# Performance work log

Hardware: AMD Instinct MI355X
Metric: run time of the kernel (lower is better)

Reference implementation:

```python
import jax, jax.numpy as jnp
import numpy as np

VOCAB = 1_000_000
TOTAL = 819_200
BATCH = 16_384
DIM = 16


def setup_inputs() -> dict:
    key = jax.random.key(0)
    k1, k2, k3, k4 = jax.random.split(key, 4)
    feature_ids = jax.random.randint(k1, (TOTAL,), 0, VOCAB, dtype=jnp.int64 if jax.config.jax_enable_x64 else jnp.int32)
    feature_ratings = jax.random.uniform(k2, (TOTAL,), dtype=jnp.float32)
    segment_ids = jnp.sort(jax.random.randint(k3, (TOTAL,), 0, BATCH))
    weight = jax.random.normal(k4, (VOCAB, DIM), dtype=jnp.float32)
    bias = jnp.zeros((DIM,), dtype=jnp.float32)
    return {
        "feature_ids": feature_ids,
        "feature_ratings": feature_ratings,
        "segment_ids": segment_ids,
        "batch_size": BATCH,
        "weight": weight,
        "bias": bias,
    }


def reference(feature_ids, feature_ratings, segment_ids, batch_size, weight, bias):
    # gather rows [total, D], weight by per-token rating, ragged segment sum
    rows = weight[feature_ids] * feature_ratings[:, None]
    summed = jax.ops.segment_sum(rows, segment_ids, num_segments=batch_size,
                                 indices_are_sorted=True)
    return summed + bias  # [batch, D]
```

## Files before the change

### kernel.cpp

```cpp
#include <hip/hip_runtime.h>

#define DIM 16
#define CHUNK 4
#define NCHUNK 8
#define K_TOK (CHUNK * NCHUNK)

__global__ void init_out_kernel(float4* __restrict__ out4,
                                const float* __restrict__ bias,
                                int n4) {
    int i = blockIdx.x * blockDim.x + threadIdx.x;
    if (i < n4) {
        int d = (i & 3) * 4;
        out4[i] = make_float4(bias[d], bias[d + 1], bias[d + 2], bias[d + 3]);
    }
}

__global__ __launch_bounds__(256) void features_linear_kernel(
    const int*   __restrict__ ids,
    const float* __restrict__ ratings,
    const int*   __restrict__ segs,
    const float* __restrict__ weight,
    float*       __restrict__ out,
    int total) {
    int tid = blockIdx.x * blockDim.x + threadIdx.x;
    int d = tid & (DIM - 1);
    int stream_id = tid >> 4;
    int t0 = stream_id * K_TOK;
    if (t0 >= total) return;

    float acc = 0.0f;
    int prev = segs[t0];

    if (t0 + K_TOK <= total) {
        const int4*   idv = (const int4*)(ids + t0);
        const float4* rv  = (const float4*)(ratings + t0);
        const int4*   sv  = (const int4*)(segs + t0);

        int4   id = idv[0];
        float4 r  = rv[0];
        int4   s  = sv[0];

        #pragma unroll
        for (int c = 0; c < NCHUNK; ++c) {
            float w0 = weight[(size_t)id.x * DIM + d];
            float w1 = weight[(size_t)id.y * DIM + d];
            float w2 = weight[(size_t)id.z * DIM + d];
            float w3 = weight[(size_t)id.w * DIM + d];

            int4 nid; float4 nr; int4 ns;
            if (c + 1 < NCHUNK) {
                nid = idv[c + 1];
                nr  = rv[c + 1];
                ns  = sv[c + 1];
            }

            if (s.x != prev) { atomicAdd(&out[prev * DIM + d], acc); acc = 0.0f; prev = s.x; }
            acc = fmaf(w0, r.x, acc);
            if (s.y != prev) { atomicAdd(&out[prev * DIM + d], acc); acc = 0.0f; prev = s.y; }
            acc = fmaf(w1, r.y, acc);
            if (s.z != prev) { atomicAdd(&out[prev * DIM + d], acc); acc = 0.0f; prev = s.z; }
            acc = fmaf(w2, r.z, acc);
            if (s.w != prev) { atomicAdd(&out[prev * DIM + d], acc); acc = 0.0f; prev = s.w; }
            acc = fmaf(w3, r.w, acc);

            id = nid; r = nr; s = ns;
        }
    } else {
        int tend = total;
        for (int t = t0; t < tend; ++t) {
            int seg = segs[t];
            if (seg != prev) {
                atomicAdd(&out[prev * DIM + d], acc);
                acc = 0.0f;
                prev = seg;
            }
            acc = fmaf(weight[(size_t)ids[t] * DIM + d], ratings[t], acc);
        }
    }
    atomicAdd(&out[prev * DIM + d], acc);
}

extern "C" void kernel_launch(void* const* d_in, const int* in_sizes, int n_in,
                              void* d_out, int out_size, void* d_ws, size_t ws_size,
                              hipStream_t stream) {
    const int*   ids     = (const int*)d_in[0];
    const float* ratings = (const float*)d_in[1];
    const int*   segs    = (const int*)d_in[2];
    const float* weight  = (const float*)d_in[4];
    const float* bias    = (const float*)d_in[5];
    float* out = (float*)d_out;

    int total = in_sizes[0];

    {
        int n4 = out_size / 4;
        int threads = 256;
        int blocks = (n4 + threads - 1) / threads;
        init_out_kernel<<<blocks, threads, 0, stream>>>((float4*)out, bias, n4);
    }

    {
        int n_streams = (total + K_TOK - 1) / K_TOK;
        long long n_threads = (long long)n_streams * DIM;
        int threads = 256;
        int blocks = (int)((n_threads + threads - 1) / threads);
        features_linear_kernel<<<blocks, threads, 0, stream>>>(
            ids, ratings, segs, weight, out, total);
    }
}
```

Measured before the change: 118.0 us.

## Use float4 row loads with 4 lanes per token stream and shorter streams

```diff
diff --git a/kernel.cpp b/kernel.cpp
--- a/kernel.cpp
+++ b/kernel.cpp
@@ -1,9 +1,8 @@
 #include <hip/hip_runtime.h>
 
 #define DIM 16
-#define CHUNK 4
-#define NCHUNK 8
-#define K_TOK (CHUNK * NCHUNK)
+#define LPS 4
+#define K_TOK 8
 
 __global__ void init_out_kernel(float4* __restrict__ out4,
                                 const float* __restrict__ bias,
@@ -23,12 +22,13 @@
     float*       __restrict__ out,
     int total) {
     int tid = blockIdx.x * blockDim.x + threadIdx.x;
-    int d = tid & (DIM - 1);
-    int stream_id = tid >> 4;
+    int j = tid & (LPS - 1);
+    int d0 = j * 4;
+    int stream_id = tid >> 2;
     int t0 = stream_id * K_TOK;
     if (t0 >= total) return;
 
-    float acc = 0.0f;
+    float4 acc = make_float4(0.f, 0.f, 0.f, 0.f);
     int prev = segs[t0];
 
     if (t0 + K_TOK <= total) {
@@ -36,48 +36,76 @@
         const float4* rv  = (const float4*)(ratings + t0);
         const int4*   sv  = (const int4*)(segs + t0);
 
-        int4   id = idv[0];
-        float4 r  = rv[0];
-        int4   s  = sv[0];
+        int4   id0 = idv[0], id1 = idv[1];
+        float4 r0  = rv[0],  r1  = rv[1];
+        int4   s0  = sv[0],  s1  = sv[1];
 
-        #pragma unroll
-        for (int c = 0; c < NCHUNK; ++c) {
-            float w0 = weight[(size_t)id.x * DIM + d];
-            float w1 = weight[(size_t)id.y * DIM + d];
-            float w2 = weight[(size_t)id.z * DIM + d];
-            float w3 = weight[(size_t)id.w * DIM + d];
+        #define WROW(idx_) (*(const float4*)(weight + (size_t)(idx_) * DIM + d0))
+        float4 w0 = WROW(id0.x);
+        float4 w1 = WROW(id0.y);
+        float4 w2 = WROW(id0.z);
+        float4 w3 = WROW(id0.w);
+        float4 w4 = WROW(id1.x);
+        float4 w5 = WROW(id1.y);
+        float4 w6 = WROW(id1.z);
+        float4 w7 = WROW(id1.w);
+        #undef WROW
 
-            int4 nid; float4 nr; int4 ns;
-            if (c + 1 < NCHUNK) {
-                nid = idv[c + 1];
-                nr  = rv[c + 1];
-                ns  = sv[c + 1];
+        #define FLUSH()                                                    \
+            {                                                              \
+                float* o = &out[prev * DIM + d0];                          \
+                atomicAdd(o + 0, acc.x);                                   \
+                atomicAdd(o + 1, acc.y);                                   \
+                atomicAdd(o + 2, acc.z);                                   \
+                atomicAdd(o + 3, acc.w);                                   \
+                acc = make_float4(0.f, 0.f, 0.f, 0.f);                     \
             }
+        #define STEP(sv_, wv_, rv_)                                        \
+            if ((sv_) != prev) { FLUSH(); prev = (sv_); }                  \
+            acc.x = fmaf((wv_).x, (rv_), acc.x);                           \
+            acc.y = fmaf((wv_).y, (rv_), acc.y);                           \
+            acc.z = fmaf((wv_).z, (rv_), acc.z);                           \
+            acc.w = fmaf((wv_).w, (rv_), acc.w);
 
-            if (s.x != prev) { atomicAdd(&out[prev * DIM + d], acc); acc = 0.0f; prev = s.x; }
-            acc = fmaf(w0, r.x, acc);
-            if (s.y != prev) { atomicAdd(&out[prev * DIM + d], acc); acc = 0.0f; prev = s.y; }
-            acc = fmaf(w1, r.y, acc);
-            if (s.z != prev) { atomicAdd(&out[prev * DIM + d], acc); acc = 0.0f; prev = s.z; }
-            acc = fmaf(w2, r.z, acc);
-            if (s.w != prev) { atomicAdd(&out[prev * DIM + d], acc); acc = 0.0f; prev = s.w; }
-            acc = fmaf(w3, r.w, acc);
+        STEP(s0.x, w0, r0.x)  STEP(s0.y, w1, r0.y)
+        STEP(s0.z, w2, r0.z)  STEP(s0.w, w3, r0.w)
+        STEP(s1.x, w4, r1.x)  STEP(s1.y, w5, r1.y)
+        STEP(s1.z, w6, r1.z)  STEP(s1.w, w7, r1.w)
 
-            id = nid; r = nr; s = ns;
+        {
+            float* o = &out[prev * DIM + d0];
+            atomicAdd(o + 0, acc.x);
+            atomicAdd(o + 1, acc.y);
+            atomicAdd(o + 2, acc.z);
+            atomicAdd(o + 3, acc.w);
         }
+        #undef STEP
+        #undef FLUSH
     } else {
-        int tend = total;
-        for (int t = t0; t < tend; ++t) {
+        for (int t = t0; t < total; ++t) {
             int seg = segs[t];
             if (seg != prev) {
-                atomicAdd(&out[prev * DIM + d], acc);
-                acc = 0.0f;
+                float* o = &out[prev * DIM + d0];
+                atomicAdd(o + 0, acc.x);
+                atomicAdd(o + 1, acc.y);
+                atomicAdd(o + 2, acc.z);
+                atomicAdd(o + 3, acc.w);
+                acc = make_float4(0.f, 0.f, 0.f, 0.f);
                 prev = seg;
             }
-            acc = fmaf(weight[(size_t)ids[t] * DIM + d], ratings[t], acc);
+            const float4 w = *(const float4*)(weight + (size_t)ids[t] * DIM + d0);
+            float r = ratings[t];
+            acc.x = fmaf(w.x, r, acc.x);
+            acc.y = fmaf(w.y, r, acc.y);
+            acc.z = fmaf(w.z, r, acc.z);
+            acc.w = fmaf(w.w, r, acc.w);
         }
+        float* o = &out[prev * DIM + d0];
+        atomicAdd(o + 0, acc.x);
+        atomicAdd(o + 1, acc.y);
+        atomicAdd(o + 2, acc.z);
+        atomicAdd(o + 3, acc.w);
     }
-    atomicAdd(&out[prev * DIM + d], acc);
 }
 
 extern "C" void kernel_launch(void* const* d_in, const int* in_sizes, int n_in,
@@ -101,7 +129,7 @@
 
     {
         int n_streams = (total + K_TOK - 1) / K_TOK;
-        long long n_threads = (long long)n_streams * DIM;
+        long long n_threads = (long long)n_streams * LPS;
         int threads = 256;
         int blocks = (int)((n_threads + threads - 1) / threads);
         features_linear_kernel<<<blocks, threads, 0, stream>>>(
```

New measurement: 131.1 us. +11.1%, slower.
